# Optimization experiments

Measured on AMD Instinct MI355X. Metric: run time of the kernel, lower is better.

## Reference

```python
import jax, jax.numpy as jnp
import numpy as np

SEQ, BATCH, D = 256, 4096, 100  # D = 2*hidden_size
STD = 0.05


def setup_inputs() -> dict:
    key = jax.random.key(0)
    k1, k2, k3, k4, k5 = jax.random.split(key, 5)
    return {
        "f_output": jax.random.normal(k1, (SEQ, BATCH, D), dtype=jnp.float32),
        "h_output": jax.random.normal(k2, (2, BATCH, D // 2), dtype=jnp.float32),
        "sentence_weight": jax.random.normal(k3, (D, D), dtype=jnp.float32) * STD,
        "sentence_bias": jax.random.normal(k4, (1, D), dtype=jnp.float32) * STD,
        "context_weight": jax.random.normal(k5, (D, 1), dtype=jnp.float32) * STD,
    }


def reference(f_output, h_output, sentence_weight, sentence_bias, context_weight):
    # matrix_mul: per-timestep mm + bias + tanh, vectorized over seq. [S,B,D]
    u = jnp.tanh(jnp.einsum('sbd,de->sbe', f_output, sentence_weight) + sentence_bias)
    # context projection (matrix_mul with no bias still applies tanh), squeeze -> [S,B]
    scores = jnp.tanh(jnp.einsum('sbd,dk->sbk', u, context_weight))[..., 0]
    # F.softmax on [B,S] defaults to dim=1 => softmax over seq
    attn = jax.nn.softmax(scores, axis=0)  # [S,B]
    # element_wise_mul: weighted sum over seq, keepdim -> [1,B,D]
    pooled = jnp.sum(f_output * attn[:, :, None], axis=0, keepdims=True)
    return (pooled, h_output)
```

## Files before the change

kernel.cpp:

```cpp
#include <hip/hip_runtime.h>
#include <hip/hip_bf16.h>

#define SEQ 256
#define BATCH 4096
#define DD 100
#define SB (BATCH * DD)
#define NBCOL 8
#define SCH 8
#define NCHUNK (SEQ / SCH)
#define ROWS (SCH * NBCOL)
#define SLAB_B (NBCOL * DD * 4)
#define CH_BYTES (ROWS * DD * 4)

typedef __attribute__((ext_vector_type(8))) short bf16x8;
typedef __attribute__((ext_vector_type(4))) float f32x4;
typedef __attribute__((ext_vector_type(4))) unsigned u32x4;

#define WAIT_VM7  asm volatile("s_waitcnt vmcnt(7)" ::: "memory")
#define WAIT_VM0  asm volatile("s_waitcnt vmcnt(0)" ::: "memory")
#define WAIT_LGKM asm volatile("s_waitcnt lgkmcnt(0)" ::: "memory")

__device__ __forceinline__ short f2bf(float x) {
    __hip_bfloat16 hv = __float2bfloat16(x);
    return *reinterpret_cast<short*>(&hv);
}
__device__ __forceinline__ float fast_tanh(float x) {
    float ax = fabsf(x);
    float e  = __expf(-2.0f * ax);
    float t  = (1.0f - e) * __builtin_amdgcn_rcpf(1.0f + e);
    return copysignf(t, x);
}
__device__ __forceinline__ float pade_tanh(float x) {
    const float x2  = x * x;
    const float num = x * (27.0f + x2);
    const float den = fmaf(9.0f, x2, 27.0f);
    const float t   = num * __builtin_amdgcn_rcpf(den);
    return fminf(1.0f, fmaxf(-1.0f, t));
}
__device__ __forceinline__ unsigned pack_bf2(float lo, float hi) {
    return __builtin_amdgcn_perm(__builtin_bit_cast(unsigned, hi),
                                 __builtin_bit_cast(unsigned, lo),
                                 0x07060302u);
}

__global__ void prep_wfrag(const float* __restrict__ W, uint4* __restrict__ wsf) {
    const int idx = blockIdx.x * 256 + threadIdx.x;
    if (idx >= 28 * 64) return;
    const int l  = idx & 63;
    const int ft = idx >> 6;
    const int t  = ft & 3;
    const int n  = ft >> 2;
    const int col   = 16 * n + (l & 15);
    const int kbase = 32 * t + 8 * (l >> 4);
    unsigned short v[8];
    #pragma unroll
    for (int e = 0; e < 8; ++e) {
        const int k = kbase + e;
        const float w = (col < DD && k < DD) ? W[k * DD + col] : 0.0f;
        v[e] = (unsigned short)f2bf(w);
    }
    uint4 u;
    u.x = (unsigned)v[0] | ((unsigned)v[1] << 16);
    u.y = (unsigned)v[2] | ((unsigned)v[3] << 16);
    u.z = (unsigned)v[4] | ((unsigned)v[5] << 16);
    u.w = (unsigned)v[6] | ((unsigned)v[7] << 16);
    wsf[ft * 64 + l] = u;
}

__device__ __forceinline__ void stage_chunk(const float* __restrict__ f,
                                            int s0, int b0, float* lbase,
                                            int wid, int lane) {
    #pragma unroll
    for (int r = 0; r < 6; ++r) {
        const int q   = wid + 4 * r;
        const int L   = (q << 10) + (lane << 4);
        const int s   = L / SLAB_B;
        const int rem = L - s * SLAB_B;
        const float* gp = f + (size_t)(s0 + s) * SB + (size_t)b0 * DD + (rem >> 2);
        __builtin_amdgcn_global_load_lds(
            (const __attribute__((address_space(1))) void*)gp,
            (__attribute__((address_space(3))) void*)((char*)lbase + L),
            16, 0, 0);
    }
    {
        const int L   = 24 * 1024 + wid * 256 + lane * 4;
        const int s   = L / SLAB_B;
        const int rem = L - s * SLAB_B;
        const float* gp = f + (size_t)(s0 + s) * SB + (size_t)b0 * DD + (rem >> 2);
        __builtin_amdgcn_global_load_lds(
            (const __attribute__((address_space(1))) void*)gp,
            (__attribute__((address_space(3))) void*)((char*)lbase + L),
            4, 0, 0);
    }
}

__global__ __launch_bounds__(256, 2)
void fused_sent_attn(const float* __restrict__ f,
                     const uint4* __restrict__ wsf,
                     const float* __restrict__ bias,
                     const float* __restrict__ cw,
                     const float* __restrict__ h,
                     float* __restrict__ out)
{
    __shared__ __align__(16) float fs[3][ROWS * DD];
    __shared__ float wexp[ROWS];
    __shared__ float den_s[NBCOL];

    const int tid  = threadIdx.x;
    const int lane = tid & 63;
    const int wid  = tid >> 6;
    const int lr   = lane & 15;
    const int g    = lane >> 4;
    const int b0   = blockIdx.x * NBCOL;

    float bias_r[7], cw_r[7];
    #pragma unroll
    for (int n = 0; n < 7; ++n) {
        const int c = 16 * n + lr;
        bias_r[n] = (c < DD) ? bias[c] : 0.0f;
        cw_r[n]   = (c < DD) ? cw[c]   : 0.0f;
    }
    {
        const size_t obase = (size_t)BATCH * DD;
        const size_t HB = (size_t)BATCH * 50;
        if (tid < 200) {
            const int half = tid / 100, rem = tid - 100 * half;
            const float4* hs = reinterpret_cast<const float4*>(h + half * HB + (size_t)b0 * 50);
            float4* od = reinterpret_cast<float4*>(out + obase + half * HB + (size_t)b0 * 50);
            od[rem] = hs[rem];
        }
    }

    bf16x8 wr[28];
    #pragma unroll
    for (int i = 0; i < 28; ++i)
        wr[i] = *reinterpret_cast<const bf16x8*>(&wsf[i * 64 + lane]);
    WAIT_VM0;

    stage_chunk(f, 0,   b0, fs[0], wid, lane);
    stage_chunk(f, SCH, b0, fs[1], wid, lane);
    WAIT_VM7;
    __builtin_amdgcn_s_barrier();
    __builtin_amdgcn_sched_barrier(0);

    const int pb = tid / 25, q4 = tid % 25;
    const bool pact = (tid < 200);
    f32x4 pacc = {0.0f, 0.0f, 0.0f, 0.0f};
    float dreg = 0.0f;

    int cur = 0;
    for (int jc = 0; jc < NCHUNK; ++jc) {
        const int nxt2 = (cur + 2 >= 3) ? cur - 1 : cur + 2;

        if (jc + 2 < NCHUNK)
            stage_chunk(f, (jc + 2) * SCH, b0, fs[nxt2], wid, lane);

        {
            const float* rp = &fs[cur][(16 * wid + lr) * DD];
            bf16x8 a[4];
            #pragma unroll
            for (int t = 0; t < 3; ++t) {
                const float4 u0 = *reinterpret_cast<const float4*>(rp + 32 * t + 8 * g);
                const float4 u1 = *reinterpret_cast<const float4*>(rp + 32 * t + 8 * g + 4);
                u32x4 pk = {pack_bf2(u0.x, u0.y), pack_bf2(u0.z, u0.w),
                            pack_bf2(u1.x, u1.y), pack_bf2(u1.z, u1.w)};
                a[t] = __builtin_bit_cast(bf16x8, pk);
            }
            {
                u32x4 pk = {0u, 0u, 0u, 0u};
                if (g == 0) {
                    const float4 u0 = *reinterpret_cast<const float4*>(rp + 96);
                    pk.x = pack_bf2(u0.x, u0.y);
                    pk.y = pack_bf2(u0.z, u0.w);
                }
                a[3] = __builtin_bit_cast(bf16x8, pk);
            }

            float scp[4] = {0, 0, 0, 0};
            #pragma unroll
            for (int n = 0; n < 7; ++n) {
                f32x4 acc = {bias_r[n], bias_r[n], bias_r[n], bias_r[n]};
                acc = __builtin_amdgcn_mfma_f32_16x16x32_bf16(a[0], wr[4 * n + 0], acc, 0, 0, 0);
                acc = __builtin_amdgcn_mfma_f32_16x16x32_bf16(a[1], wr[4 * n + 1], acc, 0, 0, 0);
                acc = __builtin_amdgcn_mfma_f32_16x16x32_bf16(a[2], wr[4 * n + 2], acc, 0, 0, 0);
                acc = __builtin_amdgcn_mfma_f32_16x16x32_bf16(a[3], wr[4 * n + 3], acc, 0, 0, 0);
                #pragma unroll
                for (int r = 0; r < 4; ++r)
                    scp[r] = fmaf(pade_tanh(acc[r]), cw_r[n], scp[r]);
            }
            #pragma unroll
            for (int r = 0; r < 4; ++r) {
                float v = scp[r];
                v += __shfl_xor(v, 1);
                v += __shfl_xor(v, 2);
                v += __shfl_xor(v, 4);
                v += __shfl_xor(v, 8);
                if (lr == 0)
                    wexp[16 * wid + 4 * g + r] = __expf(fast_tanh(v));
            }
        }
        WAIT_LGKM;
        __builtin_amdgcn_s_barrier();
        __builtin_amdgcn_sched_barrier(0);

        if (pact) {
            #pragma unroll
            for (int s = 0; s < SCH; ++s) {
                const float w = wexp[s * NBCOL + pb];
                const f32x4 v = *reinterpret_cast<const f32x4*>(
                    &fs[cur][(s * NBCOL + pb) * DD + 4 * q4]);
                pacc.x = fmaf(w, v.x, pacc.x);
                pacc.y = fmaf(w, v.y, pacc.y);
                pacc.z = fmaf(w, v.z, pacc.z);
                pacc.w = fmaf(w, v.w, pacc.w);
            }
        } else if (tid < 208) {
            const int bcol = tid - 200;
            float d = 0.0f;
            #pragma unroll
            for (int s = 0; s < SCH; ++s) d += wexp[s * NBCOL + bcol];
            dreg += d;
        }

        if (jc + 2 < NCHUNK) { WAIT_VM7; } else { WAIT_VM0; }
        __builtin_amdgcn_s_barrier();
        __builtin_amdgcn_sched_barrier(0);
        cur = (cur + 1 >= 3) ? 0 : cur + 1;
    }

    if (tid >= 200 && tid < 208) den_s[tid - 200] = dreg;
    __syncthreads();
    if (pact) {
        const float rd = 1.0f / den_s[pb];
        float4 o;
        o.x = pacc.x * rd;
        o.y = pacc.y * rd;
        o.z = pacc.z * rd;
        o.w = pacc.w * rd;
        *reinterpret_cast<float4*>(&out[(size_t)(b0 + pb) * DD + 4 * q4]) = o;
    }
}

extern "C" void kernel_launch(void* const* d_in, const int* in_sizes, int n_in,
                              void* d_out, int out_size, void* d_ws, size_t ws_size,
                              hipStream_t stream) {
    const float* f    = (const float*)d_in[0];
    const float* h    = (const float*)d_in[1];
    const float* W    = (const float*)d_in[2];
    const float* bias = (const float*)d_in[3];
    const float* cw   = (const float*)d_in[4];
    float* out = (float*)d_out;

    uint4* wsf = (uint4*)d_ws;

    prep_wfrag<<<7, 256, 0, stream>>>(W, wsf);
    fused_sent_attn<<<BATCH / NBCOL, 256, 0, stream>>>(f, wsf, bias, cw, h, out);
}
```

Before: 119.3 us.

## Accumulate pooled output from MFMA A-fragments in registers, drop mid-chunk barrier

```diff
diff --git a/kernel.cpp b/kernel.cpp
--- a/kernel.cpp
+++ b/kernel.cpp
@@ -24,6 +24,12 @@
     __hip_bfloat16 hv = __float2bfloat16(x);
     return *reinterpret_cast<short*>(&hv);
 }
+__device__ __forceinline__ float bf2f_lo(unsigned int u) {
+    return __builtin_bit_cast(float, u << 16);
+}
+__device__ __forceinline__ float bf2f_hi(unsigned int u) {
+    return __builtin_bit_cast(float, u & 0xffff0000u);
+}
 __device__ __forceinline__ float fast_tanh(float x) {
     float ax = fabsf(x);
     float e  = __expf(-2.0f * ax);
@@ -103,8 +109,7 @@
                      float* __restrict__ out)
 {
     __shared__ __align__(16) float fs[3][ROWS * DD];
-    __shared__ float wexp[ROWS];
-    __shared__ float den_s[NBCOL];
+    __shared__ uint4 wlds3[7 * 16];
 
     const int tid  = threadIdx.x;
     const int lane = tid & 63;
@@ -112,6 +117,8 @@
     const int lr   = lane & 15;
     const int g    = lane >> 4;
     const int b0   = blockIdx.x * NBCOL;
+
+    if (tid < 7 * 16) wlds3[tid] = wsf[(4 * (tid >> 4) + 3) * 64 + (tid & 15)];
 
     float bias_r[7], cw_r[7];
     #pragma unroll
@@ -130,22 +137,22 @@
             od[rem] = hs[rem];
         }
     }
-
-    bf16x8 wr[28];
-    #pragma unroll
-    for (int i = 0; i < 28; ++i)
-        wr[i] = *reinterpret_cast<const bf16x8*>(&wsf[i * 64 + lane]);
+    bf16x8 wr[21];
+    #pragma unroll
+    for (int n = 0; n < 7; ++n)
+        #pragma unroll
+        for (int t = 0; t < 3; ++t)
+            wr[3 * n + t] = *reinterpret_cast<const bf16x8*>(&wsf[(4 * n + t) * 64 + lane]);
     WAIT_VM0;
 
     stage_chunk(f, 0,   b0, fs[0], wid, lane);
     stage_chunk(f, SCH, b0, fs[1], wid, lane);
     WAIT_VM7;
+    WAIT_LGKM;
     __builtin_amdgcn_s_barrier();
     __builtin_amdgcn_sched_barrier(0);
 
-    const int pb = tid / 25, q4 = tid % 25;
-    const bool pact = (tid < 200);
-    f32x4 pacc = {0.0f, 0.0f, 0.0f, 0.0f};
+    float pacc[4][8] = {{0}};
     float dreg = 0.0f;
 
     int cur = 0;
@@ -155,71 +162,70 @@
         if (jc + 2 < NCHUNK)
             stage_chunk(f, (jc + 2) * SCH, b0, fs[nxt2], wid, lane);
 
+        const float* rp = &fs[cur][(16 * wid + lr) * DD];
+        bf16x8 a[4];
+        #pragma unroll
+        for (int t = 0; t < 3; ++t) {
+            const float4 u0 = *reinterpret_cast<const float4*>(rp + 32 * t + 8 * g);
+            const float4 u1 = *reinterpret_cast<const float4*>(rp + 32 * t + 8 * g + 4);
+            u32x4 pk = {pack_bf2(u0.x, u0.y), pack_bf2(u0.z, u0.w),
+                        pack_bf2(u1.x, u1.y), pack_bf2(u1.z, u1.w)};
+            a[t] = __builtin_bit_cast(bf16x8, pk);
+        }
         {
-            const float* rp = &fs[cur][(16 * wid + lr) * DD];
-            bf16x8 a[4];
+            u32x4 pk = {0u, 0u, 0u, 0u};
+            if (g == 0) {
+                const float4 u0 = *reinterpret_cast<const float4*>(rp + 96);
+                pk.x = pack_bf2(u0.x, u0.y);
+                pk.y = pack_bf2(u0.z, u0.w);
+            }
+            a[3] = __builtin_bit_cast(bf16x8, pk);
+        }
+
+        float scp[4] = {0, 0, 0, 0};
+        #pragma unroll
+        for (int n = 0; n < 7; ++n) {
+            bf16x8 b3 = {0, 0, 0, 0, 0, 0, 0, 0};
+            if (g == 0) b3 = *reinterpret_cast<const bf16x8*>(&wlds3[16 * n + lr]);
+            f32x4 acc = {bias_r[n], bias_r[n], bias_r[n], bias_r[n]};
+            acc = __builtin_amdgcn_mfma_f32_16x16x32_bf16(a[0], wr[3 * n + 0], acc, 0, 0, 0);
+            acc = __builtin_amdgcn_mfma_f32_16x16x32_bf16(a[1], wr[3 * n + 1], acc, 0, 0, 0);
+            acc = __builtin_amdgcn_mfma_f32_16x16x32_bf16(a[2], wr[3 * n + 2], acc, 0, 0, 0);
+            acc = __builtin_amdgcn_mfma_f32_16x16x32_bf16(a[3], b3,            acc, 0, 0, 0);
             #pragma unroll
-            for (int t = 0; t < 3; ++t) {
-                const float4 u0 = *reinterpret_cast<const float4*>(rp + 32 * t + 8 * g);
-                const float4 u1 = *reinterpret_cast<const float4*>(rp + 32 * t + 8 * g + 4);
-                u32x4 pk = {pack_bf2(u0.x, u0.y), pack_bf2(u0.z, u0.w),
-                            pack_bf2(u1.x, u1.y), pack_bf2(u1.z, u1.w)};
-                a[t] = __builtin_bit_cast(bf16x8, pk);
+            for (int r = 0; r < 4; ++r)
+                scp[r] = fmaf(pade_tanh(acc[r]), cw_r[n], scp[r]);
+        }
+        #pragma unroll
+        for (int r = 0; r < 4; ++r) {
+            float v = scp[r];
+            v += __shfl_xor(v, 1);
+            v += __shfl_xor(v, 2);
+            v += __shfl_xor(v, 4);
+            v += __shfl_xor(v, 8);
+            scp[r] = v;
+        }
+        {
+            const int src = (lr >> 2) << 4;
+            const float tt0 = __shfl(scp[0], src);
+            const float tt1 = __shfl(scp[1], src);
+            const float tt2 = __shfl(scp[2], src);
+            const float tt3 = __shfl(scp[3], src);
+            const float ta = (lr & 1) ? tt1 : tt0;
+            const float tb = (lr & 1) ? tt3 : tt2;
+            const float Srow = (lr & 2) ? tb : ta;
+            const float w = __expf(fast_tanh(Srow));
+
+            #pragma unroll
+            for (int t = 0; t < 4; ++t) {
+                const u32x4 u = __builtin_bit_cast(u32x4, a[t]);
+                #pragma unroll
+                for (int j = 0; j < 4; ++j) {
+                    pacc[t][2 * j]     = fmaf(w, bf2f_lo(u[j]), pacc[t][2 * j]);
+                    pacc[t][2 * j + 1] = fmaf(w, bf2f_hi(u[j]), pacc[t][2 * j + 1]);
+                }
             }
-            {
-                u32x4 pk = {0u, 0u, 0u, 0u};
-                if (g == 0) {
-                    const float4 u0 = *reinterpret_cast<const float4*>(rp + 96);
-                    pk.x = pack_bf2(u0.x, u0.y);
-                    pk.y = pack_bf2(u0.z, u0.w);
-                }
-                a[3] = __builtin_bit_cast(bf16x8, pk);
-            }
-
-            float scp[4] = {0, 0, 0, 0};
-            #pragma unroll
-            for (int n = 0; n < 7; ++n) {
-                f32x4 acc = {bias_r[n], bias_r[n], bias_r[n], bias_r[n]};
-                acc = __builtin_amdgcn_mfma_f32_16x16x32_bf16(a[0], wr[4 * n + 0], acc, 0, 0, 0);
-                acc = __builtin_amdgcn_mfma_f32_16x16x32_bf16(a[1], wr[4 * n + 1], acc, 0, 0, 0);
-                acc = __builtin_amdgcn_mfma_f32_16x16x32_bf16(a[2], wr[4 * n + 2], acc, 0, 0, 0);
-                acc = __builtin_amdgcn_mfma_f32_16x16x32_bf16(a[3], wr[4 * n + 3], acc, 0, 0, 0);
-                #pragma unroll
-                for (int r = 0; r < 4; ++r)
-                    scp[r] = fmaf(pade_tanh(acc[r]), cw_r[n], scp[r]);
-            }
-            #pragma unroll
-            for (int r = 0; r < 4; ++r) {
-                float v = scp[r];
-                v += __shfl_xor(v, 1);
-                v += __shfl_xor(v, 2);
-                v += __shfl_xor(v, 4);
-                v += __shfl_xor(v, 8);
-                if (lr == 0)
-                    wexp[16 * wid + 4 * g + r] = __expf(fast_tanh(v));
-            }
-        }
-        WAIT_LGKM;
-        __builtin_amdgcn_s_barrier();
-        __builtin_amdgcn_sched_barrier(0);
-
-        if (pact) {
-            #pragma unroll
-            for (int s = 0; s < SCH; ++s) {
-                const float w = wexp[s * NBCOL + pb];
-                const f32x4 v = *reinterpret_cast<const f32x4*>(
-                    &fs[cur][(s * NBCOL + pb) * DD + 4 * q4]);
-                pacc.x = fmaf(w, v.x, pacc.x);
-                pacc.y = fmaf(w, v.y, pacc.y);
-                pacc.z = fmaf(w, v.z, pacc.z);
-                pacc.w = fmaf(w, v.w, pacc.w);
-            }
-        } else if (tid < 208) {
-            const int bcol = tid - 200;
-            float d = 0.0f;
-            #pragma unroll
-            for (int s = 0; s < SCH; ++s) d += wexp[s * NBCOL + bcol];
-            dreg += d;
+            dreg += w;
         }
 
         if (jc + 2 < NCHUNK) { WAIT_VM7; } else { WAIT_VM0; }
@@ -228,15 +234,48 @@
         cur = (cur + 1 >= 3) ? 0 : cur + 1;
     }
 
-    if (tid >= 200 && tid < 208) den_s[tid - 200] = dreg;
+    float pv[4][8];
+    #pragma unroll
+    for (int t = 0; t < 4; ++t)
+        #pragma unroll
+        for (int e = 0; e < 8; ++e)
+            pv[t][e] = pacc[t][e] + __shfl_xor(pacc[t][e], 8);
+    const float dv = dreg + __shfl_xor(dreg, 8);
+
+    float* pool_sc = &fs[0][0];
+    float* den_sc  = &fs[1][0];
+    if (lr < 8) {
+        float* dst = pool_sc + (wid * 8 + lr) * 104;
+        #pragma unroll
+        for (int t = 0; t < 3; ++t) {
+            const int d0 = 32 * t + 8 * g;
+            const float4 v0 = {pv[t][0], pv[t][1], pv[t][2], pv[t][3]};
+            const float4 v1 = {pv[t][4], pv[t][5], pv[t][6], pv[t][7]};
+            *reinterpret_cast<float4*>(dst + d0)     = v0;
+            *reinterpret_cast<float4*>(dst + d0 + 4) = v1;
+        }
+        if (g == 0) {
+            const float4 v0 = {pv[3][0], pv[3][1], pv[3][2], pv[3][3]};
+            *reinterpret_cast<float4*>(dst + 96) = v0;
+            den_sc[wid * 8 + lr] = dv;
+        }
+    }
     __syncthreads();
-    if (pact) {
-        const float rd = 1.0f / den_s[pb];
+
+    if (tid < 200) {
+        const int pb = tid / 25, q4 = tid % 25;
+        f32x4 acc = {0.0f, 0.0f, 0.0f, 0.0f};
+        float den = 0.0f;
+        #pragma unroll
+        for (int w2 = 0; w2 < 4; ++w2) {
+            const f32x4 v = *reinterpret_cast<const f32x4*>(
+                pool_sc + (w2 * 8 + pb) * 104 + 4 * q4);
+            acc.x += v.x; acc.y += v.y; acc.z += v.z; acc.w += v.w;
+            den += den_sc[w2 * 8 + pb];
+        }
+        const float rd = 1.0f / den;
         float4 o;
-        o.x = pacc.x * rd;
-        o.y = pacc.y * rd;
-        o.z = pacc.z * rd;
-        o.w = pacc.w * rd;
+        o.x = acc.x * rd; o.y = acc.y * rd; o.z = acc.z * rd; o.w = acc.w * rd;
         *reinterpret_cast<float4*>(&out[(size_t)(b0 + pb) * DD + 4 * q4]) = o;
     }
 }
```

After: 106.0 us. 1.13x faster.
